# Kernel optimization log

Measured on AMD Instinct MI355X. Metric: run time of the kernel, lower is better.

## Reference

```python
import jax, jax.numpy as jnp
import numpy as np

QUERY_DIM = 256
HIDDEN_DIM = 256
NUM_HEADS = 8
HEAD_DIM = HIDDEN_DIM // NUM_HEADS
NORM_FACT = float(HIDDEN_DIM / NUM_HEADS) ** (-0.5)


def setup_inputs() -> dict:
    key = jax.random.key(0)
    ks = jax.random.split(key, 7)
    b, Q, H, W = 4, 300, 100, 100
    q = jax.random.normal(ks[0], (b, Q, QUERY_DIM), dtype=jnp.float32)
    k = jax.random.normal(ks[1], (b, QUERY_DIM, H, W), dtype=jnp.float32)
    mask = jax.random.randint(ks[2], (b, H, W), 0, 2).astype(jnp.bool_)
    # xavier_uniform for Linear(query_dim, hidden_dim): bound = sqrt(6/(fan_in+fan_out))
    bound = float(np.sqrt(6.0 / (QUERY_DIM + HIDDEN_DIM)))
    q_w = jax.random.uniform(ks[3], (HIDDEN_DIM, QUERY_DIM), jnp.float32, -bound, bound)
    k_w = jax.random.uniform(ks[4], (HIDDEN_DIM, QUERY_DIM), jnp.float32, -bound, bound)
    q_b = jnp.zeros((HIDDEN_DIM,), jnp.float32)
    k_b = jnp.zeros((HIDDEN_DIM,), jnp.float32)
    return {"q": q, "k": k, "mask": mask, "q_w": q_w, "q_b": q_b, "k_w": k_w, "k_b": k_b}


def reference(q, k, mask, q_w, q_b, k_w, k_b):
    b, Q, _ = q.shape
    _, C, H, W = k.shape
    # q_linear: [b,Q,query_dim] -> [b,Q,hidden]
    qp = jnp.einsum('bqc,hc->bqh', q, q_w) + q_b
    # k projection: 1x1 conv == channel-wise linear: [b,C,H,W] -> [b,hidden,H,W]
    kp = jnp.einsum('bchw,oc->bohw', k, k_w) + k_b[None, :, None, None]
    qh = qp.reshape(b, Q, NUM_HEADS, HEAD_DIM)
    kh = kp.reshape(b, NUM_HEADS, HEAD_DIM, H, W)
    # attention scores: [b, Q, n_heads, H, W]
    weights = jnp.einsum('bqnc,bnchw->bqnhw', qh * NORM_FACT, kh)
    if mask is not None:
        weights = jnp.where(mask[:, None, None, :, :], -jnp.inf, weights)
    # softmax over flattened (heads, H, W) — faithful to flatten(2) in the original
    flat = weights.reshape(b, Q, NUM_HEADS * H * W)
    weights = jax.nn.softmax(flat, axis=-1).reshape(b, Q, NUM_HEADS, H, W)
    return weights
```

## Files before the change

kernel.cpp:

```cpp
#include <hip/hip_runtime.h>
#include <math.h>

#define BB 4
#define QQ 300
#define CC 256
#define NH 8
#define HD 32
#define HWN 10000
#define NT 625
#define NCHUNK 125
#define TPC 5
#define QCH 4
#define NQT 5
#define MT 19
#define NORM_FACT 0.17677669529663687f

typedef __attribute__((ext_vector_type(8))) short short8_t;
typedef __attribute__((ext_vector_type(4))) float f32x4_t;
typedef __attribute__((ext_vector_type(4))) int   i32x4_t;

union FragU { uint32_t u[4]; short8_t v; };

__device__ __forceinline__ unsigned short bf16_rn(float x) {
    uint32_t u = __float_as_uint(x);
    return (unsigned short)((u + 0x7fffu + ((u >> 16) & 1u)) >> 16);
}
__device__ __forceinline__ float bf16_f(unsigned short h) {
    return __uint_as_float(((uint32_t)h) << 16);
}

__global__ void prep_kwB_kernel(const float* __restrict__ kw,
                                unsigned short* __restrict__ kwB_hi,
                                unsigned short* __restrict__ kwB_lo) {
    const int ot = blockIdx.x, ks = blockIdx.y;
    const int l = threadIdx.x;
    const int o = ot * 16 + (l & 15);
    const int c0 = ks * 32 + (l >> 4) * 8;
    const size_t base = ((size_t)(ot * 8 + ks) * 64 + l) * 8;
    #pragma unroll
    for (int j = 0; j < 8; ++j) {
        const float x = kw[o * CC + c0 + j];
        const unsigned short h = bf16_rn(x);
        kwB_hi[base + j] = h;
        kwB_lo[base + j] = bf16_rn(x - bf16_f(h));
    }
}

__global__ __launch_bounds__(256)
void qproj_kernel(const float* __restrict__ qin,
                  const unsigned short* __restrict__ qwB_hi,
                  const unsigned short* __restrict__ qwB_lo,
                  const float* __restrict__ qb,
                  unsigned short* __restrict__ qp_il) {
    const int wid = threadIdx.x >> 6, l = threadIdx.x & 63;
    const int rt = blockIdx.x;
    const int ot4 = wid;
    const int jb = (l >> 4) * 8;
    const int col = l & 15;

    FragU a_hi[8], a_lo[8];
    const float* abase = qin + ((size_t)rt * 16 + col) * CC;
    #pragma unroll
    for (int ks = 0; ks < 8; ++ks) {
        #pragma unroll
        for (int tt = 0; tt < 4; ++tt) {
            const int c = ks * 32 + jb + 2 * tt;
            const float x0 = abase[c];
            const float x1 = abase[c + 1];
            const unsigned short h0 = bf16_rn(x0), h1 = bf16_rn(x1);
            const unsigned short g0 = bf16_rn(x0 - bf16_f(h0));
            const unsigned short g1 = bf16_rn(x1 - bf16_f(h1));
            a_hi[ks].u[tt] = (uint32_t)h0 | ((uint32_t)h1 << 16);
            a_lo[ks].u[tt] = (uint32_t)g0 | ((uint32_t)g1 << 16);
        }
    }

    #pragma unroll 1
    for (int t = 0; t < 4; ++t) {
        const int ot = ot4 * 4 + t;
        f32x4_t c = {0.f, 0.f, 0.f, 0.f};
        #pragma unroll
        for (int ks = 0; ks < 8; ++ks) {
            const size_t fb = ((size_t)(ot * 8 + ks) * 64 + l) * 8;
            const short8_t bh = *reinterpret_cast<const short8_t*>(qwB_hi + fb);
            const short8_t bl = *reinterpret_cast<const short8_t*>(qwB_lo + fb);
            c = __builtin_amdgcn_mfma_f32_16x16x32_bf16(a_hi[ks].v, bh, c, 0, 0, 0);
            c = __builtin_amdgcn_mfma_f32_16x16x32_bf16(a_hi[ks].v, bl, c, 0, 0, 0);
            c = __builtin_amdgcn_mfma_f32_16x16x32_bf16(a_lo[ks].v, bh, c, 0, 0, 0);
        }
        const int o = ot * 16 + col;
        const int n = o >> 5, osub = o & 31;
        const float bias = qb[o];
        #pragma unroll
        for (int r = 0; r < 4; ++r) {
            const int row = rt * 16 + (l >> 4) * 4 + r;
            const float v = (c[r] + bias) * NORM_FACT;
            const size_t base = ((size_t)row * NH + n) * 64 + osub;
            const unsigned short h = bf16_rn(v);
            qp_il[base]      = h;
            qp_il[base + 32] = bf16_rn(v - bf16_f(h));
        }
    }
}

__global__ __launch_bounds__(256)
void kproj_kernel(const float* __restrict__ kin,
                  const unsigned short* __restrict__ kwB_hi,
                  const unsigned short* __restrict__ kwB_lo,
                  const float* __restrict__ kb,
                  unsigned short* __restrict__ kp_il) {
    __shared__ float kf[CC][17];
    const int wid = threadIdx.x >> 6, l = threadIdx.x & 63;
    const int bu  = blockIdx.x;
    const int hwt = bu % NT;
    const int b   = bu / NT;
    const int ot4 = wid;

    {
        const int tid = threadIdx.x;
        const float* kb0 = kin + (size_t)b * CC * HWN + hwt * 16;
        #pragma unroll
        for (int iter = 0; iter < 4; ++iter) {
            const int c   = iter * 64 + (tid >> 2);
            const int cl  = (tid & 3) * 4;
            const float4 v = *reinterpret_cast<const float4*>(
                kb0 + (size_t)c * HWN + cl);
            kf[c][cl]     = v.x;
            kf[c][cl + 1] = v.y;
            kf[c][cl + 2] = v.z;
            kf[c][cl + 3] = v.w;
        }
    }
    __syncthreads();

    const int jb  = (l >> 4) * 8;
    const int col = l & 15;

    f32x4_t acc[4];
    #pragma unroll
    for (int t = 0; t < 4; ++t) {
        const float bias = kb[(ot4 * 4 + t) * 16 + col];
        acc[t] = {bias, bias, bias, bias};
    }

    #pragma unroll 2
    for (int ks = 0; ks < 8; ++ks) {
        FragU a_hi, a_lo;
        #pragma unroll
        for (int tt = 0; tt < 4; ++tt) {
            const int c = ks * 32 + jb + 2 * tt;
            const float x0 = kf[c][col];
            const float x1 = kf[c + 1][col];
            const unsigned short h0 = bf16_rn(x0), h1 = bf16_rn(x1);
            const unsigned short g0 = bf16_rn(x0 - bf16_f(h0));
            const unsigned short g1 = bf16_rn(x1 - bf16_f(h1));
            a_hi.u[tt] = (uint32_t)h0 | ((uint32_t)h1 << 16);
            a_lo.u[tt] = (uint32_t)g0 | ((uint32_t)g1 << 16);
        }
        #pragma unroll
        for (int t = 0; t < 4; ++t) {
            const int ot = ot4 * 4 + t;
            const size_t fb = ((size_t)(ot * 8 + ks) * 64 + l) * 8;
            const short8_t bh = *reinterpret_cast<const short8_t*>(kwB_hi + fb);
            const short8_t bl = *reinterpret_cast<const short8_t*>(kwB_lo + fb);
            acc[t] = __builtin_amdgcn_mfma_f32_16x16x32_bf16(a_hi.v, bh, acc[t], 0, 0, 0);
            acc[t] = __builtin_amdgcn_mfma_f32_16x16x32_bf16(a_hi.v, bl, acc[t], 0, 0, 0);
            acc[t] = __builtin_amdgcn_mfma_f32_16x16x32_bf16(a_lo.v, bh, acc[t], 0, 0, 0);
        }
    }

    #pragma unroll
    for (int t = 0; t < 4; ++t) {
        const int o = (ot4 * 4 + t) * 16 + col;
        const int n = o >> 5, osub = o & 31;
        #pragma unroll
        for (int r = 0; r < 4; ++r) {
            const int hwrow = hwt * 16 + (l >> 4) * 4 + r;
            const size_t base = ((size_t)(b * HWN + hwrow) * NH + n) * 64 + osub;
            const float v = acc[t][r];
            const unsigned short h = bf16_rn(v);
            kp_il[base]      = h;
            kp_il[base + 32] = bf16_rn(v - bf16_f(h));
        }
    }
}

__global__ __launch_bounds__(256)
void attn_stats_kernel(const unsigned short* __restrict__ qp_il,
                       const unsigned short* __restrict__ kp_il,
                       const int* __restrict__ mask,
                       float* __restrict__ partials) {
    const int wid = threadIdx.x >> 6, l = threadIdx.x & 63;
    const int wu = blockIdx.x * 4 + wid;
    const int qh = wu & 1;
    int tmp = wu >> 1;
    const int ch = tmp % NCHUNK; tmp /= NCHUNK;
    const int n = tmp & 7;
    const int b = tmp >> 3;

    short8_t ah[TPC], al[TPC];
    float mf[TPC][4];
    #pragma unroll
    for (int t = 0; t < TPC; ++t) {
        const int tile = ch * TPC + t;
        const int hwr = tile * 16 + (l & 15);
        const size_t abase = ((size_t)(b * HWN + hwr) * NH + n) * 64 + (l >> 4) * 8;
        ah[t] = *reinterpret_cast<const short8_t*>(kp_il + abase);
        al[t] = *reinterpret_cast<const short8_t*>(kp_il + abase + 32);
        const int hw4 = tile * 16 + (l >> 4) * 4;
        const i32x4_t mv = *reinterpret_cast<const i32x4_t*>(mask + b * HWN + hw4);
        mf[t][0] = mv.x ? 0.f : 1.f;
        mf[t][1] = mv.y ? 0.f : 1.f;
        mf[t][2] = mv.z ? 0.f : 1.f;
        mf[t][3] = mv.w ? 0.f : 1.f;
    }

    const int qt0 = qh * 10;
    const int qt1 = qh ? MT : 10;
    #pragma unroll 2
    for (int qt = qt0; qt < qt1; ++qt) {
        const int qa = qt * 16 + (l & 15);
        const int qcl = qa < QQ ? qa : QQ - 1;
        const size_t bbase = ((size_t)(b * QQ + qcl) * NH + n) * 64 + (l >> 4) * 8;
        const short8_t bh = *reinterpret_cast<const short8_t*>(qp_il + bbase);
        const short8_t bl = *reinterpret_cast<const short8_t*>(qp_il + bbase + 32);

        float a = 0.f;
        #pragma unroll
        for (int t = 0; t < TPC; ++t) {
            f32x4_t c = {0.f, 0.f, 0.f, 0.f};
            c = __builtin_amdgcn_mfma_f32_16x16x32_bf16(ah[t], bh, c, 0, 0, 0);
            c = __builtin_amdgcn_mfma_f32_16x16x32_bf16(ah[t], bl, c, 0, 0, 0);
            c = __builtin_amdgcn_mfma_f32_16x16x32_bf16(al[t], bh, c, 0, 0, 0);
            a += __expf(c[0]) * mf[t][0] + __expf(c[1]) * mf[t][1]
               + __expf(c[2]) * mf[t][2] + __expf(c[3]) * mf[t][3];
        }
        a += __shfl_xor(a, 16, 64);
        a += __shfl_xor(a, 32, 64);
        if (l < 16) {
            const int qr = qt * 16 + l;
            if (qr < QQ)
                partials[(((size_t)b * QQ + qr) * NH + n) * NCHUNK + ch] = a;
        }
    }
}

__global__ void invsum_kernel(const float* __restrict__ partials,
                              float* __restrict__ invS) {
    const int row = blockIdx.x;
    const int l = threadIdx.x;
    float s = 0.f;
    const float* p = partials + (size_t)row * (NH * NCHUNK);
    for (int i = l; i < NH * NCHUNK; i += 64) s += p[i];
    #pragma unroll
    for (int m = 1; m < 64; m <<= 1) s += __shfl_xor(s, m, 64);
    if (l == 0) invS[row] = 1.0f / s;
}

__global__ __launch_bounds__(256)
void attn_out_kernel(const unsigned short* __restrict__ qp_il,
                     const unsigned short* __restrict__ kp_il,
                     const int* __restrict__ mask,
                     const float* __restrict__ invS,
                     float* __restrict__ out) {
    const int wid = threadIdx.x >> 6, l = threadIdx.x & 63;
    const int wu = blockIdx.x * 4 + wid;
    const int ch = wu % NCHUNK;
    int tmp = wu / NCHUNK;
    const int qc = tmp % QCH; tmp /= QCH;
    const int n = tmp & 7;
    const int b = tmp >> 3;

    short8_t bh[NQT], bl[NQT];
    float isv[NQT];
    float* optr[NQT];
    bool qok[NQT];
    #pragma unroll
    for (int tt = 0; tt < NQT; ++tt) {
        const int qa = (qc * NQT + tt) * 16 + (l & 15);
        const int qcl = qa < QQ ? qa : QQ - 1;
        qok[tt] = qa < QQ;
        const size_t bbase = ((size_t)(b * QQ + qcl) * NH + n) * 64 + (l >> 4) * 8;
        bh[tt] = *reinterpret_cast<const short8_t*>(qp_il + bbase);
        bl[tt] = *reinterpret_cast<const short8_t*>(qp_il + bbase + 32);
        isv[tt] = invS[b * QQ + qcl];
        optr[tt] = out + (((size_t)b * QQ + qcl) * NH + n) * HWN;
    }

    #pragma unroll
    for (int t = 0; t < TPC; ++t) {
        const int tile = ch * TPC + t;
        const int hwr = tile * 16 + (l & 15);
        const size_t abase = ((size_t)(b * HWN + hwr) * NH + n) * 64 + (l >> 4) * 8;
        const short8_t ah = *reinterpret_cast<const short8_t*>(kp_il + abase);
        const short8_t al = *reinterpret_cast<const short8_t*>(kp_il + abase + 32);
        const int hw4 = tile * 16 + (l >> 4) * 4;
        const i32x4_t mv = *reinterpret_cast<const i32x4_t*>(mask + b * HWN + hw4);
        const float m0 = mv.x ? 0.f : 1.f, m1 = mv.y ? 0.f : 1.f;
        const float m2 = mv.z ? 0.f : 1.f, m3 = mv.w ? 0.f : 1.f;
        #pragma unroll
        for (int tt = 0; tt < NQT; ++tt) {
            f32x4_t c = {0.f, 0.f, 0.f, 0.f};
            c = __builtin_amdgcn_mfma_f32_16x16x32_bf16(ah, bh[tt], c, 0, 0, 0);
            c = __builtin_amdgcn_mfma_f32_16x16x32_bf16(ah, bl[tt], c, 0, 0, 0);
            c = __builtin_amdgcn_mfma_f32_16x16x32_bf16(al, bh[tt], c, 0, 0, 0);
            const float is = isv[tt];
            f32x4_t rv;
            rv[0] = __expf(c[0]) * is * m0;
            rv[1] = __expf(c[1]) * is * m1;
            rv[2] = __expf(c[2]) * is * m2;
            rv[3] = __expf(c[3]) * is * m3;
            if (qok[tt])
                __builtin_nontemporal_store(rv,
                    reinterpret_cast<f32x4_t*>(optr[tt] + hw4));
        }
    }
}

extern "C" void kernel_launch(void* const* d_in, const int* in_sizes, int n_in,
                              void* d_out, int out_size, void* d_ws, size_t ws_size,
                              hipStream_t stream) {
    const float* q    = (const float*)d_in[0];
    const float* k    = (const float*)d_in[1];
    const int*   mask = (const int*)d_in[2];
    const float* qw   = (const float*)d_in[3];
    const float* qb   = (const float*)d_in[4];
    const float* kw   = (const float*)d_in[5];
    const float* kb   = (const float*)d_in[6];
    float* out = (float*)d_out;

    char* wsb = (char*)d_ws;
    unsigned short* kp_il = (unsigned short*)wsb;
    unsigned short* qp_il = (unsigned short*)(wsb + 40960000);
    float* invS           = (float*)(wsb + 40960000 + 1228800);

    unsigned short* kwB_hi = (unsigned short*)d_out;
    unsigned short* kwB_lo = kwB_hi + 65536;
    unsigned short* qwB_hi = kwB_hi + 131072;
    unsigned short* qwB_lo = kwB_hi + 196608;
    float* partials = (float*)((char*)d_out + (4u << 20));

    prep_kwB_kernel<<<dim3(16, 8), 64, 0, stream>>>(kw, kwB_hi, kwB_lo);
    prep_kwB_kernel<<<dim3(16, 8), 64, 0, stream>>>(qw, qwB_hi, qwB_lo);
    qproj_kernel<<<75, 256, 0, stream>>>(q, qwB_hi, qwB_lo, qb, qp_il);
    kproj_kernel<<<BB * NT, 256, 0, stream>>>(k, kwB_hi, kwB_lo, kb, kp_il);
    attn_stats_kernel<<<(BB * NH * NCHUNK * 2) / 4, 256, 0, stream>>>(
        qp_il, kp_il, mask, partials);
    invsum_kernel<<<BB * QQ, 64, 0, stream>>>(partials, invS);
    attn_out_kernel<<<(BB * NH * QCH * NCHUNK) / 4, 256, 0, stream>>>(
        qp_il, kp_il, mask, invS, out);
}
```

Baseline: 219.3 us.

## Stage attention output tiles in LDS for fully coalesced row stores

Each wave of the output kernel now handles one 16-query tile and a 256-wide hw chunk instead of five query tiles over 80 hw positions. The results go into a swizzled shared-memory buffer and are then written back row by row as contiguous 1KB segments, where before each store was a scattered 16-byte write. This targets write coalescing on the dominant output stream, which is about 384MB. In exchange the kernel uses 64KB of LDS per block, which limits occupancy, and it reloads the kp fragments once per query tile with no reuse across query tiles.

```diff
diff --git a/kernel.cpp b/kernel.cpp
--- a/kernel.cpp
+++ b/kernel.cpp
@@ -10,9 +10,8 @@
 #define NT 625
 #define NCHUNK 125
 #define TPC 5
-#define QCH 4
-#define NQT 5
 #define MT 19
+#define OCH 40
 #define NORM_FACT 0.17677669529663687f
 
 typedef __attribute__((ext_vector_type(8))) short short8_t;
@@ -263,33 +262,28 @@
                      const int* __restrict__ mask,
                      const float* __restrict__ invS,
                      float* __restrict__ out) {
+    __shared__ float obuf[4][16][256];
     const int wid = threadIdx.x >> 6, l = threadIdx.x & 63;
     const int wu = blockIdx.x * 4 + wid;
-    const int ch = wu % NCHUNK;
-    int tmp = wu / NCHUNK;
-    const int qc = tmp % QCH; tmp /= QCH;
+    const int ch = wu % OCH;
+    int tmp = wu / OCH;
+    const int qt = tmp % MT; tmp /= MT;
     const int n = tmp & 7;
     const int b = tmp >> 3;
 
-    short8_t bh[NQT], bl[NQT];
-    float isv[NQT];
-    float* optr[NQT];
-    bool qok[NQT];
-    #pragma unroll
-    for (int tt = 0; tt < NQT; ++tt) {
-        const int qa = (qc * NQT + tt) * 16 + (l & 15);
-        const int qcl = qa < QQ ? qa : QQ - 1;
-        qok[tt] = qa < QQ;
-        const size_t bbase = ((size_t)(b * QQ + qcl) * NH + n) * 64 + (l >> 4) * 8;
-        bh[tt] = *reinterpret_cast<const short8_t*>(qp_il + bbase);
-        bl[tt] = *reinterpret_cast<const short8_t*>(qp_il + bbase + 32);
-        isv[tt] = invS[b * QQ + qcl];
-        optr[tt] = out + (((size_t)b * QQ + qcl) * NH + n) * HWN;
-    }
-
-    #pragma unroll
-    for (int t = 0; t < TPC; ++t) {
-        const int tile = ch * TPC + t;
+    const int qa = qt * 16 + (l & 15);
+    const int qcl = qa < QQ ? qa : QQ - 1;
+    const size_t bbase = ((size_t)(b * QQ + qcl) * NH + n) * 64 + (l >> 4) * 8;
+    const short8_t bh = *reinterpret_cast<const short8_t*>(qp_il + bbase);
+    const short8_t bl = *reinterpret_cast<const short8_t*>(qp_il + bbase + 32);
+    const float is = invS[b * QQ + qcl];
+
+    const int ntile = (ch == OCH - 1) ? 1 : 16;
+    const int q_lane = l & 15;
+    const int xorq = (q_lane & 7) << 2;
+
+    for (int t = 0; t < ntile; ++t) {
+        const int tile = ch * 16 + t;
         const int hwr = tile * 16 + (l & 15);
         const size_t abase = ((size_t)(b * HWN + hwr) * NH + n) * 64 + (l >> 4) * 8;
         const short8_t ah = *reinterpret_cast<const short8_t*>(kp_il + abase);
@@ -298,21 +292,32 @@
         const i32x4_t mv = *reinterpret_cast<const i32x4_t*>(mask + b * HWN + hw4);
         const float m0 = mv.x ? 0.f : 1.f, m1 = mv.y ? 0.f : 1.f;
         const float m2 = mv.z ? 0.f : 1.f, m3 = mv.w ? 0.f : 1.f;
-        #pragma unroll
-        for (int tt = 0; tt < NQT; ++tt) {
-            f32x4_t c = {0.f, 0.f, 0.f, 0.f};
-            c = __builtin_amdgcn_mfma_f32_16x16x32_bf16(ah, bh[tt], c, 0, 0, 0);
-            c = __builtin_amdgcn_mfma_f32_16x16x32_bf16(ah, bl[tt], c, 0, 0, 0);
-            c = __builtin_amdgcn_mfma_f32_16x16x32_bf16(al, bh[tt], c, 0, 0, 0);
-            const float is = isv[tt];
-            f32x4_t rv;
-            rv[0] = __expf(c[0]) * is * m0;
-            rv[1] = __expf(c[1]) * is * m1;
-            rv[2] = __expf(c[2]) * is * m2;
-            rv[3] = __expf(c[3]) * is * m3;
-            if (qok[tt])
-                __builtin_nontemporal_store(rv,
-                    reinterpret_cast<f32x4_t*>(optr[tt] + hw4));
+
+        f32x4_t c = {0.f, 0.f, 0.f, 0.f};
+        c = __builtin_amdgcn_mfma_f32_16x16x32_bf16(ah, bh, c, 0, 0, 0);
+        c = __builtin_amdgcn_mfma_f32_16x16x32_bf16(ah, bl, c, 0, 0, 0);
+        c = __builtin_amdgcn_mfma_f32_16x16x32_bf16(al, bh, c, 0, 0, 0);
+        f32x4_t rv;
+        rv[0] = __expf(c[0]) * is * m0;
+        rv[1] = __expf(c[1]) * is * m1;
+        rv[2] = __expf(c[2]) * is * m2;
+        rv[3] = __expf(c[3]) * is * m3;
+
+        const int col = (t * 16 + ((l >> 4) << 2)) ^ xorq;
+        *reinterpret_cast<f32x4_t*>(&obuf[wid][q_lane][col]) = rv;
+    }
+
+    const int nhw = ntile * 16;
+    const int hwbase = ch * 256;
+    #pragma unroll 4
+    for (int qi = 0; qi < 16; ++qi) {
+        const int q = qt * 16 + qi;
+        if (q >= QQ) break;
+        if (l * 4 < nhw) {
+            const int rcol = (l * 4) ^ ((qi & 7) << 2);
+            const f32x4_t v = *reinterpret_cast<const f32x4_t*>(&obuf[wid][qi][rcol]);
+            __builtin_nontemporal_store(v, reinterpret_cast<f32x4_t*>(
+                out + (((size_t)b * QQ + q) * NH + n) * HWN + hwbase + l * 4));
         }
     }
 }
@@ -347,6 +352,6 @@
     attn_stats_kernel<<<(BB * NH * NCHUNK * 2) / 4, 256, 0, stream>>>(
         qp_il, kp_il, mask, partials);
     invsum_kernel<<<BB * QQ, 64, 0, stream>>>(partials, invS);
-    attn_out_kernel<<<(BB * NH * QCH * NCHUNK) / 4, 256, 0, stream>>>(
+    attn_out_kernel<<<(BB * NH * MT * OCH) / 4, 256, 0, stream>>>(
         qp_il, kp_il, mask, invS, out);
 }
```

New measurement: 242.7 us. 1.11x slower.
